# Performance work log

Hardware: AMD Instinct MI355X
Metric: run time of the kernel (lower is better)

## Reference

```python
import jax, jax.numpy as jnp
import numpy as np

BATCH, IN_DIM, GRID, OUT_DIM = 2048, 512, 32, 512


def setup_inputs() -> dict:
    key = jax.random.key(0)
    k_x, k_c = jax.random.split(key)
    x = jax.random.normal(k_x, (BATCH, IN_DIM), dtype=jnp.float32)
    fourier_coeffs = jax.random.normal(k_c, (2, IN_DIM, GRID, OUT_DIM), dtype=jnp.float32) / np.sqrt(GRID * OUT_DIM)
    bias = jnp.zeros((1, OUT_DIM), dtype=jnp.float32)
    return {"x": x, "fourier_coeffs": fourier_coeffs, "bias": bias}


def reference(x, fourier_coeffs, bias):
    # freqs: 1..GRID, shape (GRID,)
    freqs = jnp.arange(1, GRID + 1, dtype=x.dtype)
    kx = x[..., None] * freqs            # [B, I, G]
    cos_t = jnp.cos(kx)
    sin_t = jnp.sin(kx)
    # Equivalent to broadcast-multiply with coeffs then sum over grid and input dims:
    y = (jnp.einsum('big,igo->bo', cos_t, fourier_coeffs[0])
         + jnp.einsum('big,igo->bo', sin_t, fourier_coeffs[1]))
    return y + bias
```

## Files before the change

kernel.cpp:

```cpp
#include <hip/hip_runtime.h>
#include <hip/hip_bf16.h>
#include <stdint.h>

namespace {

constexpr int IDIM   = 512;
constexpr int ODIM   = 512;
constexpr int KTOT   = 32768;
constexpr int BM = 128, BN = 128, BK = 64;
constexpr int SPLITK = 8;
constexpr int KCHUNK = KTOT / SPLITK;
constexpr int NSTEP  = KCHUNK / BK;

typedef short    bf16x8 __attribute__((ext_vector_type(8)));
typedef float    f32x4  __attribute__((ext_vector_type(4)));
typedef float    f32x2  __attribute__((ext_vector_type(2)));
typedef uint32_t u32x4  __attribute__((ext_vector_type(4)));

__device__ __forceinline__ uint32_t f2bf1(float f) {
  union { float f; uint32_t u; } v; v.f = f;
  return (v.u + 0x7fffu + ((v.u >> 16) & 1u)) >> 16;
}
__device__ __forceinline__ uint32_t pk2(float lo, float hi) {
  return f2bf1(lo) | (f2bf1(hi) << 16);
}

__device__ __forceinline__ void gload_lds16(const void* gsrc, const char* ldsdst) {
  __builtin_amdgcn_global_load_lds(
      (const __attribute__((address_space(1))) uint32_t*)(uintptr_t)gsrc,
      (__attribute__((address_space(3))) uint32_t*)(uint32_t)(uintptr_t)ldsdst,
      16, 0, 0);
}

__global__ __launch_bounds__(256) void transpose_convert_kernel(const float* __restrict__ fc,
                                                                uint16_t* __restrict__ wt) {
  const int t = threadIdx.x, lane = t & 63, wave = t >> 6;
  const int bid = blockIdx.x;
  const int ot = bid & 3;
  const int kt = bid >> 2;
  const int o0 = ot * 128 + lane * 2;
  const int kb = kt * 128 + wave * 32;
  const float* src = fc + (size_t)kb * ODIM + o0;
  uint32_t w0[16], w1[16];
#pragma unroll
  for (int p = 0; p < 16; ++p) {
    f32x2 a = *(const f32x2*)(src + (size_t)(2 * p) * ODIM);
    f32x2 b = *(const f32x2*)(src + (size_t)(2 * p + 1) * ODIM);
    w0[p] = pk2(a.x, b.x);
    w1[p] = pk2(a.y, b.y);
  }
  uint16_t* dst0 = wt + (size_t)o0 * KTOT + kb;
  uint16_t* dst1 = dst0 + KTOT;
#pragma unroll
  for (int c = 0; c < 4; ++c) {
    *(u32x4*)(dst0 + c * 8) = *(const u32x4*)&w0[c * 4];
    *(u32x4*)(dst1 + c * 8) = *(const u32x4*)&w1[c * 4];
  }
}

__global__ __launch_bounds__(256) void init_bias_kernel(const float* __restrict__ bias,
                                                        float* __restrict__ out) {
  int i = blockIdx.x * 256 + threadIdx.x;
  ((f32x4*)out)[i] = ((const f32x4*)bias)[i & 127];
}

__global__ __launch_bounds__(256, 2) void fkan_gemm_kernel(const float* __restrict__ x,
                                                           const uint16_t* __restrict__ wt,
                                                           float* __restrict__ out) {
  __shared__ char lds[65536];

  const int t    = threadIdx.x;
  const int lane = t & 63;
  const int wave = t >> 6;

  int bid = blockIdx.x;
  int swz = (bid & 7) * 64 + (bid >> 3);
  const int bm = swz & 15;
  const int bn = (swz >> 4) & 3;
  const int bz = swz >> 6;

  const int row0  = bm * BM;
  const int col0  = bn * BN;
  const int kc0   = bz * KCHUNK;
  const int sflag = bz >> 2;
  const int ibase = (bz & 3) * 128;

  const int gr   = t & 127;
  const int ioff = t >> 7;
  const float* xp = x + (size_t)(row0 + gr) * IDIM + ibase + ioff;
  int awoff[4];
#pragma unroll
  for (int j = 0; j < 4; ++j)
    awoff[j] = gr * 128 + (((ioff * 4 + j) ^ (gr & 7)) << 4);

  const uint16_t* wsrc[4];
  int wdst[4];
#pragma unroll
  for (int q = 0; q < 4; ++q) {
    int nl   = q * 32 + wave * 8 + (lane >> 3);
    int slot = lane & 7;
    wsrc[q] = wt + (size_t)(col0 + nl) * KTOT + kc0 + ((slot ^ (nl & 7)) << 3);
    wdst[q] = q * 4096 + wave * 1024;
  }

  const int wm = wave >> 1, wn = wave & 1;
  int arow[4], ar7[4], bcol[4], bc7[4];
#pragma unroll
  for (int m = 0; m < 4; ++m) {
    int rr = wm * 64 + m * 16 + (lane & 15);
    arow[m] = rr * 128; ar7[m] = rr & 7;
    int cc = wn * 64 + m * 16 + (lane & 15);
    bcol[m] = cc * 128; bc7[m] = cc & 7;
  }

  f32x4 acc[4][4] = {};

  auto stageW = [&](int buf, int st) {
#pragma unroll
    for (int q = 0; q < 4; ++q)
      gload_lds16(wsrc[q] + st * BK, lds + 32768 + buf * 16384 + wdst[q]);
  };

  auto genA = [&](int buf, float ang) {
    float sv, cv;
    __sincosf(ang, &sv, &cv);
    const float c2 = 2.f * cv;
    float pm1 = sflag ? 0.f : 1.f;
    float p   = sflag ? sv  : cv;
    char* ab = lds + buf * 16384;
#pragma unroll
    for (int grp = 0; grp < 4; ++grp) {
      u32x4 w;
#pragma unroll
      for (int u = 0; u < 4; ++u) {
        float a0 = p; float nx = c2 * p - pm1; pm1 = p; p = nx;
        float a1 = p; nx = c2 * p - pm1; pm1 = p; p = nx;
        w[u] = pk2(a0, a1);
      }
      *(u32x4*)(ab + awoff[grp]) = w;
    }
  };

  auto compute = [&](int buf) {
    const char* ab = lds + buf * 16384;
    const char* wb = lds + 32768 + buf * 16384;
#pragma unroll
    for (int ks = 0; ks < 2; ++ks) {
      const int ksb = ks * 4 + (lane >> 4);
      bf16x8 af[4], bfr[4];
#pragma unroll
      for (int m = 0; m < 4; ++m)
        af[m] = *(const bf16x8*)(ab + arow[m] + ((ksb ^ ar7[m]) << 4));
#pragma unroll
      for (int n = 0; n < 4; ++n)
        bfr[n] = *(const bf16x8*)(wb + bcol[n] + ((ksb ^ bc7[n]) << 4));
#pragma unroll
      for (int m = 0; m < 4; ++m)
#pragma unroll
        for (int n = 0; n < 4; ++n)
          acc[m][n] = __builtin_amdgcn_mfma_f32_16x16x32_bf16(af[m], bfr[n], acc[m][n], 0, 0, 0);
    }
  };

  float ang0 = xp[0];
  stageW(0, 0);
  genA(0, ang0);
  float angN = xp[2];
  __syncthreads();

  int cur = 0;
  for (int st = 0; st < NSTEP; ++st) {
    if (st + 1 < NSTEP) {
      float aU = angN;
      int pf = (st + 2 < NSTEP) ? (st + 2) : (NSTEP - 1);
      angN = xp[2 * pf];
      stageW(cur ^ 1, st + 1);
      genA(cur ^ 1, aU);
    }
    compute(cur);
    __syncthreads();
    cur ^= 1;
  }

#pragma unroll
  for (int m = 0; m < 4; ++m) {
#pragma unroll
    for (int n = 0; n < 4; ++n) {
      int rr = row0 + wm * 64 + m * 16 + ((lane >> 4) << 2);
      int cc = col0 + wn * 64 + n * 16 + (lane & 15);
#pragma unroll
      for (int j = 0; j < 4; ++j)
        atomicAdd(out + (size_t)(rr + j) * ODIM + cc, acc[m][n][j]);
    }
  }
}

}

extern "C" void kernel_launch(void* const* d_in, const int* in_sizes, int n_in,
                              void* d_out, int out_size, void* d_ws, size_t ws_size,
                              hipStream_t stream) {
  const float* x    = (const float*)d_in[0];
  const float* fc   = (const float*)d_in[1];
  const float* bias = (const float*)d_in[2];
  float*    out = (float*)d_out;
  uint16_t* wt  = (uint16_t*)d_ws;

  transpose_convert_kernel<<<1024, 256, 0, stream>>>(fc, wt);
  init_bias_kernel<<<1024, 256, 0, stream>>>(bias, out);
  fkan_gemm_kernel<<<512, 256, 0, stream>>>(x, wt, out);
}
```

Measured before the change: 209.6 us.

## Triple-buffer weight tiles with explicit waitcnt and speed up A-tile generation

The weight tile pipeline moves from double to triple buffering, with LDS grown to hold three W buffers. Loads are issued two steps ahead, and `__syncthreads` is replaced by explicit `s_waitcnt vmcnt`/`lgkmcnt` plus a raw barrier, so in-flight global-to-LDS loads can overlap more compute. The cos/sin generator now runs two interleaved Chebyshev recurrences (odd and even harmonics), which shortens the serial dependency chain. It also uses a cheaper perm-based bf16 pack that rounds half-up instead of round-to-nearest-even, a small precision change. The extra LDS may limit occupancy.

```diff
diff --git a/kernel.cpp b/kernel.cpp
--- a/kernel.cpp
+++ b/kernel.cpp
@@ -25,12 +25,21 @@
   return f2bf1(lo) | (f2bf1(hi) << 16);
 }
 
+__device__ __forceinline__ uint32_t pk2f(float lo, float hi) {
+  union { float f; uint32_t u; } a, b; a.f = lo; b.f = hi;
+  return __builtin_amdgcn_perm(b.u + 0x8000u, a.u + 0x8000u, 0x07060302u);
+}
+
 __device__ __forceinline__ void gload_lds16(const void* gsrc, const char* ldsdst) {
   __builtin_amdgcn_global_load_lds(
       (const __attribute__((address_space(1))) uint32_t*)(uintptr_t)gsrc,
       (__attribute__((address_space(3))) uint32_t*)(uint32_t)(uintptr_t)ldsdst,
       16, 0, 0);
 }
+
+#define WAIT_LGKM0   asm volatile("s_waitcnt lgkmcnt(0)" ::: "memory")
+#define WAIT_VM(N)   asm volatile("s_waitcnt vmcnt(" #N ")" ::: "memory")
+#define FENCE        asm volatile("" ::: "memory")
 
 __global__ __launch_bounds__(256) void transpose_convert_kernel(const float* __restrict__ fc,
                                                                 uint16_t* __restrict__ wt) {
@@ -67,7 +76,7 @@
 __global__ __launch_bounds__(256, 2) void fkan_gemm_kernel(const float* __restrict__ x,
                                                            const uint16_t* __restrict__ wt,
                                                            float* __restrict__ out) {
-  __shared__ char lds[65536];
+  __shared__ char lds[81920];
 
   const int t    = threadIdx.x;
   const int lane = t & 63;
@@ -93,13 +102,13 @@
   for (int j = 0; j < 4; ++j)
     awoff[j] = gr * 128 + (((ioff * 4 + j) ^ (gr & 7)) << 4);
 
-  const uint16_t* wsrc[4];
+  const uint16_t* wptr[4];
   int wdst[4];
 #pragma unroll
   for (int q = 0; q < 4; ++q) {
     int nl   = q * 32 + wave * 8 + (lane >> 3);
     int slot = lane & 7;
-    wsrc[q] = wt + (size_t)(col0 + nl) * KTOT + kc0 + ((slot ^ (nl & 7)) << 3);
+    wptr[q] = wt + (size_t)(col0 + nl) * KTOT + kc0 + ((slot ^ (nl & 7)) << 3);
     wdst[q] = q * 4096 + wave * 1024;
   }
 
@@ -115,35 +124,41 @@
 
   f32x4 acc[4][4] = {};
 
-  auto stageW = [&](int buf, int st) {
-#pragma unroll
-    for (int q = 0; q < 4; ++q)
-      gload_lds16(wsrc[q] + st * BK, lds + 32768 + buf * 16384 + wdst[q]);
+  auto stageW = [&](int buf) {
+#pragma unroll
+    for (int q = 0; q < 4; ++q) {
+      gload_lds16(wptr[q], lds + 32768 + buf * 16384 + wdst[q]);
+      wptr[q] += BK;
+    }
   };
 
-  auto genA = [&](int buf, float ang) {
-    float sv, cv;
-    __sincosf(ang, &sv, &cv);
-    const float c2 = 2.f * cv;
-    float pm1 = sflag ? 0.f : 1.f;
-    float p   = sflag ? sv  : cv;
-    char* ab = lds + buf * 16384;
+  auto genA = [&](int abuf, float ang) {
+    float s1, c1;
+    __sincosf(ang, &s1, &c1);
+    const float c2 = 2.f * c1 * c1 - 1.f;
+    const float s2 = 2.f * s1 * c1;
+    const float k2 = 2.f * c2;
+    float po  = sflag ? s1   : c1;
+    float pe  = sflag ? s2   : c2;
+    float pom = sflag ? -s1  : c1;
+    float pem = sflag ? 0.f  : 1.f;
+    char* ab = lds + abuf * 16384;
 #pragma unroll
     for (int grp = 0; grp < 4; ++grp) {
       u32x4 w;
 #pragma unroll
       for (int u = 0; u < 4; ++u) {
-        float a0 = p; float nx = c2 * p - pm1; pm1 = p; p = nx;
-        float a1 = p; nx = c2 * p - pm1; pm1 = p; p = nx;
-        w[u] = pk2(a0, a1);
+        w[u] = pk2f(po, pe);
+        float no = k2 * po - pom; pom = po; po = no;
+        float ne = k2 * pe - pem; pem = pe; pe = ne;
       }
       *(u32x4*)(ab + awoff[grp]) = w;
     }
   };
 
-  auto compute = [&](int buf) {
-    const char* ab = lds + buf * 16384;
-    const char* wb = lds + 32768 + buf * 16384;
+  auto compute = [&](int wbuf, int abuf) {
+    const char* ab = lds + abuf * 16384;
+    const char* wb = lds + 32768 + wbuf * 16384;
 #pragma unroll
     for (int ks = 0; ks < 2; ++ks) {
       const int ksb = ks * 4 + (lane >> 4);
@@ -162,24 +177,37 @@
     }
   };
 
-  float ang0 = xp[0];
-  stageW(0, 0);
-  genA(0, ang0);
-  float angN = xp[2];
-  __syncthreads();
-
-  int cur = 0;
+  float angCur  = xp[0];
+  float angNext = xp[2];
+  stageW(0);
+  stageW(1);
+  genA(0, angCur);
+  WAIT_VM(4);
+  WAIT_LGKM0;
+  __builtin_amdgcn_s_barrier();
+  FENCE;
+
+  int wb_c = 0;
+  int ws_c = 2;
   for (int st = 0; st < NSTEP; ++st) {
+    const int ab = st & 1;
+    if (st + 2 < NSTEP) {
+      stageW(ws_c);
+      ws_c = (ws_c == 2) ? 0 : ws_c + 1;
+    }
     if (st + 1 < NSTEP) {
-      float aU = angN;
-      int pf = (st + 2 < NSTEP) ? (st + 2) : (NSTEP - 1);
-      angN = xp[2 * pf];
-      stageW(cur ^ 1, st + 1);
-      genA(cur ^ 1, aU);
-    }
-    compute(cur);
-    __syncthreads();
-    cur ^= 1;
+      float a = angNext;
+      if (st + 2 < NSTEP) angNext = xp[2 * (st + 2)];
+      genA(ab ^ 1, a);
+    }
+    compute(wb_c, ab);
+    wb_c = (wb_c == 2) ? 0 : wb_c + 1;
+    if (st + 1 < NSTEP) {
+      WAIT_LGKM0;
+      if (st + 2 < NSTEP) { WAIT_VM(4); } else { WAIT_VM(0); }
+      __builtin_amdgcn_s_barrier();
+      FENCE;
+    }
   }
 
 #pragma unroll
```

Measured after the change: 198.7 us. -5.2%, faster.
